# Kernel tuning notes

Measured on AMD Instinct MI355X. Metric: run time of the kernel, lower is better.

Reference implementation:

```python
import jax, jax.numpy as jnp
import numpy as np

NTYPES = 2
MAXNEI = 100
MNT = MAXNEI * NTYPES  # max_neighbor * ntypes = 200
RMIN = 0.5
RMAX = 6.0
M1 = 100   # last embedding width
M2 = 16
FH = 240   # fitting hidden width
NPHYS = 4
TFEAT = 8
B, NAT = 4, 1024


def mlp_resnet(x, Ws, bs):
    # DeepMD-style MLP: tanh layers with identity / duplicated-identity resnet
    for W, b in zip(Ws, bs):
        h = jnp.tanh(x @ W + b)
        if h.shape[-1] == x.shape[-1]:
            h = h + x
        elif h.shape[-1] == 2 * x.shape[-1]:
            h = h + jnp.concatenate([x, x], axis=-1)
        x = h
    return x


def setup_inputs() -> dict:
    key = jax.random.key(0)
    ks = jax.random.split(key, 24)
    r = jax.random.uniform(ks[0], (B, NAT, MNT), minval=0.1, maxval=7.0)
    pad = jax.random.uniform(ks[1], (B, NAT, MNT)) < 0.25
    r = jnp.where(pad, 0.0, r)
    d = jax.random.normal(ks[2], (B, NAT, MNT, 3))
    d = d / jnp.linalg.norm(d, axis=-1, keepdims=True)
    ImageDR = jnp.concatenate([r[..., None], r[..., None] * d], axis=-1).astype(jnp.float32)

    list_neigh = jax.random.randint(ks[3], (B, NAT, MNT), 0, MAXNEI)
    Imagetype_map = jax.random.randint(ks[4], (NAT,), 0, NTYPES).astype(jnp.int32)
    type_map = jnp.array([3, 14], dtype=jnp.int64)

    davg = (0.1 * jax.random.normal(ks[5], (NTYPES, MNT, 4))).astype(jnp.float32)
    dstd = (1.0 + 0.1 * jax.random.uniform(ks[6], (NTYPES, MNT, 4))).astype(jnp.float32)

    def w(k, shape):
        return (jax.random.normal(k, shape) / np.sqrt(shape[-2] if len(shape) > 1 else 1.0)).astype(jnp.float32)

    type_vector = jax.random.normal(ks[7], (NTYPES, NPHYS)).astype(jnp.float32)
    tW0 = w(ks[8], (NPHYS, TFEAT)); tb0 = jnp.zeros((TFEAT,), jnp.float32)
    eW0 = w(ks[9], (1 + TFEAT, 25)); eb0 = jnp.zeros((25,), jnp.float32)
    eW1 = w(ks[10], (25, 50));       eb1 = jnp.zeros((50,), jnp.float32)
    eW2 = w(ks[11], (50, M1));       eb2 = jnp.zeros((M1,), jnp.float32)
    fW0 = w(ks[12], (NTYPES, M2 * M1, FH)); fb0 = jnp.zeros((NTYPES, FH), jnp.float32)
    fW1 = w(ks[13], (NTYPES, FH, FH));      fb1 = jnp.zeros((NTYPES, FH), jnp.float32)
    fW2 = w(ks[14], (NTYPES, FH, FH));      fb2 = jnp.zeros((NTYPES, FH), jnp.float32)
    fWf = w(ks[15], (NTYPES, FH, 1))
    energy_shift = jnp.array([-3.2, -5.1], jnp.float32).reshape(NTYPES, 1)
    fbf = (0.01 * jax.random.normal(ks[16], (NTYPES, 1))).astype(jnp.float32) + energy_shift

    return dict(list_neigh=list_neigh, Imagetype_map=Imagetype_map, type_map=type_map,
                ImageDR=ImageDR, nghost=0, davg=davg, dstd=dstd, type_vector=type_vector,
                tW0=tW0, tb0=tb0, eW0=eW0, eb0=eb0, eW1=eW1, eb1=eb1, eW2=eW2, eb2=eb2,
                fW0=fW0, fb0=fb0, fW1=fW1, fb1=fb1, fW2=fW2, fb2=fb2, fWf=fWf, fbf=fbf)


def _forward(ImageDR, davg, dstd, type_vector, tW0, tb0, eW0, eb0, eW1, eb1, eW2, eb2,
             fW0, fb0, fW1, fb1, fW2, fb2, fWf, fbf, Imagetype_map):
    r = ImageDR[..., 0]
    r_safe = jnp.where(r > 1e-5, r, 1.0)
    inv_r = 1.0 / r_safe
    u = (r - RMIN) / (RMAX - RMIN)
    s_mid = inv_r * (u ** 3 * (-6.0 * u ** 2 + 15.0 * u - 10.0) + 1.0)
    Srij = jnp.where((r > 0) & (r < RMIN), inv_r,
                     jnp.where((r >= RMIN) & (r < RMAX), s_mid, 0.0))  # (B,N,J)
    mask = (jnp.abs(r) > 1e-5)[..., None]
    Ri = jnp.concatenate([Srij[..., None],
                          jnp.where(mask, Srij[..., None] * ImageDR[..., 1:4] * inv_r[..., None], 0.0)],
                         axis=-1)  # (B,N,J,4)
    # per-atom-type normalization
    Ri = (Ri - davg[Imagetype_map][None]) / dstd[Imagetype_map][None]

    # neighbor type feature from type-embedding net
    nt_idx = jnp.arange(MNT) // MAXNEI              # (J,) neighbor slot -> type
    tfeat = mlp_resnet(type_vector, [tW0], [tb0])   # (ntypes, TFEAT)
    nf = jnp.broadcast_to(tfeat[nt_idx][None, None], Ri.shape[:3] + (TFEAT,))
    x = jnp.concatenate([Ri[..., 0:1], nf], axis=-1)            # (B,N,J,1+TFEAT)
    G = mlp_resnet(x, [eW0, eW1, eW2], [eb0, eb1, eb2])         # (B,N,J,M1)

    xyz = jnp.einsum('bnjd,bnjm->bndm', Ri, G) / MNT            # (B,N,4,M1)
    DR = jnp.einsum('bndm,bndq->bnmq', xyz, xyz[..., :M2])      # (B,N,M1,M2)
    DR = DR.reshape(DR.shape[0], DR.shape[1], M1 * M2)

    Ei = jnp.zeros(DR.shape[:2], DR.dtype)
    for t in range(NTYPES):  # per-type fitting nets
        h = mlp_resnet(DR, [fW0[t], fW1[t], fW2[t]], [fb0[t], fb1[t], fb2[t]])
        e = (h @ fWf[t] + fbf[t])[..., 0]
        Ei = jnp.where(Imagetype_map[None, :] == t, e, Ei)
    Etot = jnp.sum(Ei, axis=1, keepdims=True)  # (B,1)
    return Etot, Ei


def reference(list_neigh, Imagetype_map, type_map, ImageDR, nghost, davg, dstd, type_vector,
              tW0, tb0, eW0, eb0, eW1, eb1, eW2, eb2,
              fW0, fb0, fW1, fb1, fW2, fb2, fWf, fbf):
    # list_neigh/type_map/nghost only participate in force computation (is_calc_f=False path)
    return _forward(ImageDR, davg, dstd, type_vector, tW0, tb0, eW0, eb0, eW1, eb1, eW2, eb2,
                    fW0, fb0, fW1, fb1, fW2, fb2, fWf, fbf, Imagetype_map)
```

## Files before the change

kernel.cpp:

```cpp
#include <hip/hip_runtime.h>
#include <hip/hip_bf16.h>

#define NATC  1024
#define BATCH 4
#define MNTC  200
#define M1C   100
#define M2C   16
#define FHC   240
#define KPAD  256
#define HSTR  264
#define H1STR 40
#define H2STR 72

typedef __attribute__((ext_vector_type(8))) short bf16x8;
typedef __attribute__((ext_vector_type(4))) float f32x4;

__device__ __forceinline__ float fast_tanh(float x){
    float e = __expf(2.0f * x);
    float r = __fdividef(1.0f, e + 1.0f);
    return fmaf(-2.0f, r, 1.0f);
}

__device__ __forceinline__ unsigned short f2bf(float x){
    __hip_bfloat16 h = __float2bfloat16(x);
    return *reinterpret_cast<unsigned short*>(&h);
}

__device__ __forceinline__ float bf2f(unsigned short u){
    unsigned int v = ((unsigned int)u) << 16;
    return *reinterpret_cast<float*>(&v);
}

__device__ __forceinline__ unsigned int pack2(float a, float b){
    return (unsigned int)f2bf(a) | ((unsigned int)f2bf(b) << 16);
}

__global__ __launch_bounds__(256) void part_kernel(const int* __restrict__ tmap,
                                                   int* __restrict__ idx,
                                                   int* __restrict__ counts){
    __shared__ int s0[256], s1[256];
    const int tid = threadIdx.x;
    int ty[4]; int c0 = 0, c1 = 0;
    #pragma unroll
    for (int r = 0; r < 4; ++r){
        ty[r] = tmap[tid*4 + r];
        if (ty[r] == 0) c0++; else c1++;
    }
    s0[tid] = c0; s1[tid] = c1;
    __syncthreads();
    for (int off = 1; off < 256; off <<= 1){
        int v0 = (tid >= off) ? s0[tid-off] : 0;
        int v1 = (tid >= off) ? s1[tid-off] : 0;
        __syncthreads();
        s0[tid] += v0; s1[tid] += v1;
        __syncthreads();
    }
    int e0 = s0[tid] - c0, e1 = s1[tid] - c1;
    #pragma unroll
    for (int r = 0; r < 4; ++r){
        int n = tid*4 + r;
        if (ty[r] == 0) idx[e0++] = n; else idx[NATC + e1++] = n;
    }
    if (tid == 255){ counts[0] = s0[255]; counts[1] = s1[255]; }
}

__global__ __launch_bounds__(256) void transp_kernel(const float* __restrict__ src,
                                                     unsigned short* __restrict__ dst,
                                                     int K, int N, int Kpad, int nkt, int nnt){
    __shared__ float tile[64][65];
    const int tid = threadIdx.x;
    int bid = blockIdx.x;
    const int t  = bid / (nkt*nnt);
    bid -= t*nkt*nnt;
    const int kt = bid / nnt;
    const int nt = bid - kt*nnt;
    const float* s = src + (size_t)t*K*N;
    unsigned short* d = dst + (size_t)t*N*Kpad;

    const int c  = tid & 63;
    const int rg = tid >> 6;
    #pragma unroll
    for (int p = 0; p < 16; ++p){
        int row = p*4 + rg;
        int gr = kt*64 + row, gc = nt*64 + c;
        tile[row][c] = (gr < K && gc < N) ? s[(size_t)gr*N + gc] : 0.0f;
    }
    __syncthreads();
    const int nn0 = tid >> 3;
    const int k8  = (tid & 7) * 8;
    #pragma unroll
    for (int p = 0; p < 2; ++p){
        int nn = p*32 + nn0;
        int gn = nt*64 + nn;
        int gk = kt*64 + k8;
        if (gn < N && gk < Kpad){
            unsigned short v[8];
            #pragma unroll
            for (int j = 0; j < 8; ++j) v[j] = f2bf(tile[k8+j][nn]);
            *(bf16x8*)(d + (size_t)gn*Kpad + gk) = *(bf16x8*)v;
        }
    }
}

__global__ __launch_bounds__(256) void prep_kernel(const float* __restrict__ tv,
                                                   const float* __restrict__ tW0,
                                                   const float* __restrict__ tb0,
                                                   const float* __restrict__ eW1,
                                                   const float* __restrict__ eW2,
                                                   unsigned short* __restrict__ ew1t,
                                                   unsigned short* __restrict__ ew2t,
                                                   float* __restrict__ tf_g){
    const int tid = threadIdx.x;
    if (tid < 16){
        int t = tid >> 3, f = tid & 7;
        float s = tb0[f];
        #pragma unroll
        for (int p = 0; p < 4; ++p) s = fmaf(tv[t*4+p], tW0[p*8+f], s);
        tf_g[tid] = fast_tanh(s) + tv[t*4 + (f & 3)];
    }
    for (int i = tid; i < 112*64; i += 256){
        int n = i >> 6, k = i & 63;
        ew2t[i] = (n < M1C && k < 50) ? f2bf(eW2[(size_t)k*M1C + n]) : (unsigned short)0;
    }
    for (int i = tid; i < 64*32; i += 256){
        int n = i >> 5, k = i & 31;
        ew1t[i] = (n < 50 && k < 25) ? f2bf(eW1[(size_t)k*50 + n]) : (unsigned short)0;
    }
}

__global__ __launch_bounds__(256, 2) void embed_kernel(
    const float4* __restrict__ imdr,
    const float4* __restrict__ davg,
    const float4* __restrict__ dstd,
    const int*    __restrict__ tmap,
    const float*  __restrict__ tf_g,
    const float*  __restrict__ eW0,
    const float*  __restrict__ eb0,
    const float*  __restrict__ eb1,
    const float*  __restrict__ eb2,
    const unsigned short* __restrict__ ew1t,
    const unsigned short* __restrict__ ew2t,
    unsigned short* __restrict__ DRout)
{
    __shared__ __align__(16) float Rif[256][4];
    __shared__ __align__(16) unsigned short H1s[256][H1STR];
    __shared__ __align__(16) unsigned short H2s[256][H2STR];

    const int tid = threadIdx.x;
    const int a   = blockIdx.x;
    const int n0  = a & (NATC - 1);
    const int itype = tmap[n0];
    const int j = tid;

    {
        unsigned int* rowp = (unsigned int*)&H1s[j][0];
        if (j < MNTC){
            float4 dr = imdr[(size_t)a*MNTC + j];
            float r  = dr.x;
            float rs = (r > 1e-5f) ? r : 1.0f;
            float ir = __fdividef(1.0f, rs);
            float u  = (r - 0.5f) * (1.0f/5.5f);
            float u2 = u*u, u3 = u2*u;
            float smid = ir * (u3 * (-6.0f*u2 + 15.0f*u - 10.0f) + 1.0f);
            float S = 0.0f;
            if (r > 0.0f && r < 0.5f)       S = ir;
            else if (r >= 0.5f && r < 6.0f) S = smid;
            bool msk = fabsf(r) > 1e-5f;
            float R0 = S;
            float R1 = msk ? S * dr.y * ir : 0.0f;
            float R2 = msk ? S * dr.z * ir : 0.0f;
            float R3 = msk ? S * dr.w * ir : 0.0f;
            float4 av = davg[itype*MNTC + j];
            float4 sv = dstd[itype*MNTC + j];
            float rin0 = __fdividef(R0 - av.x, sv.x);
            float rin1 = __fdividef(R1 - av.y, sv.y);
            float rin2 = __fdividef(R2 - av.z, sv.z);
            float rin3 = __fdividef(R3 - av.w, sv.w);
            Rif[j][0] = rin0; Rif[j][1] = rin1; Rif[j][2] = rin2; Rif[j][3] = rin3;

            float xf[8];
            const int tb = (j >= 100) ? 8 : 0;
            #pragma unroll
            for (int f = 0; f < 8; ++f) xf[f] = tf_g[tb + f];

            float h1[25];
            #pragma unroll
            for (int o = 0; o < 25; ++o) h1[o] = fmaf(rin0, eW0[o], eb0[o]);
            #pragma unroll
            for (int k = 0; k < 8; ++k){
                float hv = xf[k];
                #pragma unroll
                for (int o = 0; o < 25; ++o) h1[o] = fmaf(hv, eW0[(k+1)*25 + o], h1[o]);
            }
            #pragma unroll
            for (int o = 0; o < 25; ++o) h1[o] = fast_tanh(h1[o]);

            #pragma unroll
            for (int c = 0; c < 12; ++c) rowp[c] = pack2(h1[2*c], h1[2*c+1]);
            rowp[12] = (unsigned int)f2bf(h1[24]);
            #pragma unroll
            for (int c = 13; c < 20; ++c) rowp[c] = 0u;
        } else {
            Rif[j][0] = 0.0f; Rif[j][1] = 0.0f; Rif[j][2] = 0.0f; Rif[j][3] = 0.0f;
            #pragma unroll
            for (int c = 0; c < 20; ++c) rowp[c] = 0u;
        }
    }
    __syncthreads();

    const int lane = tid & 63;
    const int w    = tid >> 6;
    const int lc   = lane & 15;
    const int lg   = lane >> 4;

    #pragma unroll
    for (int mi = 0; mi < 4; ++mi){
        const int mt = w + mi*4;
        bf16x8 af = *(const bf16x8*)&H1s[mt*16 + lc][lg*8];
        const int rbase = mt*16 + lg*4;
        #pragma unroll
        for (int nt = 0; nt < 4; ++nt){
            const int n = nt*16 + lc;
            const bool live = (n < 50);
            float bv = live ? eb1[n] : 0.0f;
            f32x4 c;
            c[0] = bv; c[1] = bv; c[2] = bv; c[3] = bv;
            bf16x8 bfr = *(const bf16x8*)(ew1t + n*32 + lg*8);
            c = __builtin_amdgcn_mfma_f32_16x16x32_bf16(af, bfr, c, 0, 0, 0);
            const int rc = n % 25;
            #pragma unroll
            for (int i = 0; i < 4; ++i){
                const int row = rbase + i;
                unsigned short v = 0;
                if (live) v = f2bf(fast_tanh(c[i]) + bf2f(H1s[row][rc]));
                H2s[row][n] = v;
            }
        }
    }
    __syncthreads();

    float* xyzp = (float*)&H1s[0][0];
    float* xyzs = xyzp + 4*4*112;

    float bias[7];
    #pragma unroll
    for (int nt = 0; nt < 7; ++nt){
        int cg = nt*16 + lc;
        bias[nt] = (cg < M1C) ? eb2[cg] : 0.0f;
    }

    float xacc[7][4];
    #pragma unroll
    for (int nt = 0; nt < 7; ++nt)
        #pragma unroll
        for (int d = 0; d < 4; ++d) xacc[nt][d] = 0.0f;

    #pragma unroll
    for (int mi = 0; mi < 4; ++mi){
        const int mt = w + mi*4;
        const int rbase = mt*16 + lg*4;
        float4 rj[4];
        #pragma unroll
        for (int i = 0; i < 4; ++i) rj[i] = *(const float4*)&Rif[rbase + i][0];
        const unsigned short* arow = &H2s[mt*16 + lc][0];
        bf16x8 a0 = *(const bf16x8*)(arow + lg*8);
        bf16x8 a1 = *(const bf16x8*)(arow + 32 + lg*8);
        #pragma unroll
        for (int nt = 0; nt < 7; ++nt){
            const unsigned short* bp = ew2t + (size_t)(nt*16 + lc)*64 + lg*8;
            bf16x8 b0 = *(const bf16x8*)(bp);
            bf16x8 b1 = *(const bf16x8*)(bp + 32);
            f32x4 c;
            c[0] = bias[nt]; c[1] = bias[nt]; c[2] = bias[nt]; c[3] = bias[nt];
            c = __builtin_amdgcn_mfma_f32_16x16x32_bf16(a0, b0, c, 0, 0, 0);
            c = __builtin_amdgcn_mfma_f32_16x16x32_bf16(a1, b1, c, 0, 0, 0);
            const int cg = nt*16 + lc;
            const int rc = (cg >= 100) ? cg - 100 : ((cg >= 50) ? cg - 50 : cg);
            #pragma unroll
            for (int i = 0; i < 4; ++i){
                float g = fast_tanh(c[i]) + bf2f(H2s[rbase + i][rc]);
                xacc[nt][0] = fmaf(g, rj[i].x, xacc[nt][0]);
                xacc[nt][1] = fmaf(g, rj[i].y, xacc[nt][1]);
                xacc[nt][2] = fmaf(g, rj[i].z, xacc[nt][2]);
                xacc[nt][3] = fmaf(g, rj[i].w, xacc[nt][3]);
            }
        }
    }
    #pragma unroll
    for (int nt = 0; nt < 7; ++nt){
        #pragma unroll
        for (int d = 0; d < 4; ++d){
            float v = xacc[nt][d];
            v += __shfl_xor(v, 16);
            v += __shfl_xor(v, 32);
            if (lane < 16) xyzp[((w*4 + d)*112) + nt*16 + lc] = v;
        }
    }
    __syncthreads();

    for (int i = tid; i < 4*112; i += 256){
        int d = i / 112, m = i - d*112;
        xyzs[d*112 + m] = (xyzp[(0*4+d)*112 + m] + xyzp[(1*4+d)*112 + m] +
                           xyzp[(2*4+d)*112 + m] + xyzp[(3*4+d)*112 + m])
                          * (1.0f / (float)MNTC);
    }
    __syncthreads();

    for (int i = tid; i < M1C*M2C; i += 256){
        int m = i >> 4, q = i & 15;
        float s = 0.0f;
        #pragma unroll
        for (int d = 0; d < 4; ++d) s = fmaf(xyzs[d*112 + m], xyzs[d*112 + q], s);
        DRout[(size_t)a*(M1C*M2C) + i] = f2bf(s);
    }
}

__global__ __launch_bounds__(512) void fitm_kernel(
    const unsigned short* __restrict__ DRbf,
    const int*   __restrict__ idx,
    const int*   __restrict__ counts,
    const unsigned short* __restrict__ w0t,
    const unsigned short* __restrict__ w1t,
    const unsigned short* __restrict__ w2t,
    const float* __restrict__ fb0,
    const float* __restrict__ fb1,
    const float* __restrict__ fb2,
    const float* __restrict__ fWf,
    const float* __restrict__ fbf,
    float* __restrict__ out)
{
    const int bid = blockIdx.x;
    const int g = bid & 63;
    const int t = (bid >> 6) & 1;
    const int b = bid >> 7;
    const int cnt  = counts[t];
    const int base = g * 16;
    if (base >= cnt) return;
    const int na = min(16, cnt - base);

    __shared__ int ns[16];
    __shared__ __align__(16) unsigned short hA[16][HSTR];
    __shared__ __align__(16) unsigned short hB[16][HSTR];
    __shared__ float epart[8][16];

    const int tid  = threadIdx.x;
    const int lane = tid & 63;
    const int w    = tid >> 6;
    if (tid < 16) ns[tid] = idx[t*NATC + base + ((tid < na) ? tid : 0)];
    __syncthreads();

    const int lc = lane & 15;
    const int lg = lane >> 4;

    int   ncol[2];  bool act[2];  float bias0[2];
    #pragma unroll
    for (int nt = 0; nt < 2; ++nt){
        ncol[nt] = w*32 + nt*16 + lc;
        act[nt]  = (w*32 + nt*16) < FHC;
        bias0[nt] = act[nt] ? fb0[t*FHC + ncol[nt]] : 0.0f;
    }

    const unsigned short* aptr0 = DRbf + ((size_t)(b*NATC + ns[lc]))*1600 + lg*8;
    const unsigned short* bptr0[2];
    #pragma unroll
    for (int nt = 0; nt < 2; ++nt)
        bptr0[nt] = act[nt] ? (w0t + ((size_t)(t*FHC + ncol[nt]))*1600 + lg*8) : w0t;

    f32x4 acc[2];
    #pragma unroll
    for (int nt = 0; nt < 2; ++nt){
        acc[nt][0] = bias0[nt]; acc[nt][1] = bias0[nt];
        acc[nt][2] = bias0[nt]; acc[nt][3] = bias0[nt];
    }
    #pragma unroll 4
    for (int ks = 0; ks < 50; ++ks){
        bf16x8 af = *(const bf16x8*)(aptr0 + ks*32);
        #pragma unroll
        for (int nt = 0; nt < 2; ++nt){
            if (act[nt]){
                bf16x8 bfg = *(const bf16x8*)(bptr0[nt] + ks*32);
                acc[nt] = __builtin_amdgcn_mfma_f32_16x16x32_bf16(af, bfg, acc[nt], 0, 0, 0);
            }
        }
    }
    float h0r[2][4];
    #pragma unroll
    for (int nt = 0; nt < 2; ++nt){
        #pragma unroll
        for (int i = 0; i < 4; ++i){
            int row = lg*4 + i;
            if (act[nt]){
                h0r[nt][i] = fast_tanh(acc[nt][i]);
                hA[row][ncol[nt]] = f2bf(h0r[nt][i]);
            } else {
                h0r[nt][i] = 0.0f;
                hA[row][ncol[nt]] = 0;
            }
        }
    }
    __syncthreads();

    f32x4 acc1[2];
    #pragma unroll
    for (int nt = 0; nt < 2; ++nt){
        float bv = act[nt] ? fb1[t*FHC + ncol[nt]] : 0.0f;
        acc1[nt][0] = bv; acc1[nt][1] = bv; acc1[nt][2] = bv; acc1[nt][3] = bv;
    }
    const unsigned short* b1p[2];
    #pragma unroll
    for (int nt = 0; nt < 2; ++nt)
        b1p[nt] = act[nt] ? (w1t + ((size_t)(t*FHC + ncol[nt]))*KPAD + lg*8) : w1t;
    #pragma unroll
    for (int ks = 0; ks < 8; ++ks){
        bf16x8 af = *(const bf16x8*)&hA[lc][ks*32 + lg*8];
        #pragma unroll
        for (int nt = 0; nt < 2; ++nt){
            if (act[nt]){
                bf16x8 bfg = *(const bf16x8*)(b1p[nt] + ks*32);
                acc1[nt] = __builtin_amdgcn_mfma_f32_16x16x32_bf16(af, bfg, acc1[nt], 0, 0, 0);
            }
        }
    }
    float h1r[2][4];
    #pragma unroll
    for (int nt = 0; nt < 2; ++nt){
        #pragma unroll
        for (int i = 0; i < 4; ++i){
            int row = lg*4 + i;
            if (act[nt]){
                h1r[nt][i] = fast_tanh(acc1[nt][i]) + h0r[nt][i];
                hB[row][ncol[nt]] = f2bf(h1r[nt][i]);
            } else {
                h1r[nt][i] = 0.0f;
                hB[row][ncol[nt]] = 0;
            }
        }
    }
    __syncthreads();

    f32x4 acc2[2];
    #pragma unroll
    for (int nt = 0; nt < 2; ++nt){
        float bv = act[nt] ? fb2[t*FHC + ncol[nt]] : 0.0f;
        acc2[nt][0] = bv; acc2[nt][1] = bv; acc2[nt][2] = bv; acc2[nt][3] = bv;
    }
    const unsigned short* b2p[2];
    #pragma unroll
    for (int nt = 0; nt < 2; ++nt)
        b2p[nt] = act[nt] ? (w2t + ((size_t)(t*FHC + ncol[nt]))*KPAD + lg*8) : w2t;
    #pragma unroll
    for (int ks = 0; ks < 8; ++ks){
        bf16x8 af = *(const bf16x8*)&hB[lc][ks*32 + lg*8];
        #pragma unroll
        for (int nt = 0; nt < 2; ++nt){
            if (act[nt]){
                bf16x8 bfg = *(const bf16x8*)(b2p[nt] + ks*32);
                acc2[nt] = __builtin_amdgcn_mfma_f32_16x16x32_bf16(af, bfg, acc2[nt], 0, 0, 0);
            }
        }
    }

    float p0 = 0.0f, p1 = 0.0f, p2 = 0.0f, p3 = 0.0f;
    #pragma unroll
    for (int nt = 0; nt < 2; ++nt){
        if (act[nt]){
            float wfv = fWf[t*FHC + ncol[nt]];
            float h;
            h = fast_tanh(acc2[nt][0]) + h1r[nt][0]; p0 = fmaf(h, wfv, p0);
            h = fast_tanh(acc2[nt][1]) + h1r[nt][1]; p1 = fmaf(h, wfv, p1);
            h = fast_tanh(acc2[nt][2]) + h1r[nt][2]; p2 = fmaf(h, wfv, p2);
            h = fast_tanh(acc2[nt][3]) + h1r[nt][3]; p3 = fmaf(h, wfv, p3);
        }
    }
    #pragma unroll
    for (int off = 1; off < 16; off <<= 1){
        p0 += __shfl_xor(p0, off);
        p1 += __shfl_xor(p1, off);
        p2 += __shfl_xor(p2, off);
        p3 += __shfl_xor(p3, off);
    }
    if (lc == 0){
        epart[w][lg*4 + 0] = p0;
        epart[w][lg*4 + 1] = p1;
        epart[w][lg*4 + 2] = p2;
        epart[w][lg*4 + 3] = p3;
    }
    __syncthreads();
    if (tid < 16){
        float e = fbf[t];
        #pragma unroll
        for (int ww = 0; ww < 8; ++ww) e += epart[ww][tid];
        float ee = 0.0f;
        if (tid < na){
            out[4 + b*NATC + ns[tid]] = e;
            ee = e;
        }
        #pragma unroll
        for (int off = 8; off >= 1; off >>= 1) ee += __shfl_down(ee, off, 16);
        if (tid == 0) atomicAdd(&out[b], ee);
    }
}

extern "C" void kernel_launch(void* const* d_in, const int* in_sizes, int n_in,
                              void* d_out, int out_size, void* d_ws, size_t ws_size,
                              hipStream_t stream)
{
    (void)in_sizes; (void)n_in; (void)out_size; (void)ws_size;
    const int*   tmap = (const int*)d_in[1];
    const float* imdr = (const float*)d_in[3];
    const float* davg = (const float*)d_in[5];
    const float* dstd = (const float*)d_in[6];
    const float* tv   = (const float*)d_in[7];
    const float* tW0  = (const float*)d_in[8];
    const float* tb0  = (const float*)d_in[9];
    const float* eW0  = (const float*)d_in[10];
    const float* eb0  = (const float*)d_in[11];
    const float* eW1  = (const float*)d_in[12];
    const float* eb1  = (const float*)d_in[13];
    const float* eW2  = (const float*)d_in[14];
    const float* eb2  = (const float*)d_in[15];
    const float* fW0  = (const float*)d_in[16];
    const float* fb0  = (const float*)d_in[17];
    const float* fW1  = (const float*)d_in[18];
    const float* fb1  = (const float*)d_in[19];
    const float* fW2  = (const float*)d_in[20];
    const float* fb2  = (const float*)d_in[21];
    const float* fWf  = (const float*)d_in[22];
    const float* fbf  = (const float*)d_in[23];
    float* out = (float*)d_out;

    char* ws = (char*)d_ws;
    int*   counts = (int*)ws;
    int*   idx    = (int*)(ws + 64);
    unsigned short* DRbf = (unsigned short*)(ws + 16384);
    unsigned short* w0t  = DRbf + (size_t)BATCH*NATC*1600;
    unsigned short* w1t  = w0t + (size_t)2*FHC*1600;
    unsigned short* w2t  = w1t + (size_t)2*FHC*KPAD;
    unsigned short* ew2t = w2t + (size_t)2*FHC*KPAD;
    unsigned short* ew1t = ew2t + 112*64;
    float* tf_g          = (float*)(ew1t + 64*32);

    hipMemsetAsync(d_out, 0, 4*sizeof(float), stream);
    part_kernel<<<1, 256, 0, stream>>>(tmap, idx, counts);
    prep_kernel<<<1, 256, 0, stream>>>(tv, tW0, tb0, eW1, eW2, ew1t, ew2t, tf_g);
    transp_kernel<<<2*25*4, 256, 0, stream>>>(fW0, w0t, 1600, FHC, 1600, 25, 4);
    transp_kernel<<<2*4*4,  256, 0, stream>>>(fW1, w1t, FHC, FHC, KPAD, 4, 4);
    transp_kernel<<<2*4*4,  256, 0, stream>>>(fW2, w2t, FHC, FHC, KPAD, 4, 4);
    embed_kernel<<<BATCH*NATC, 256, 0, stream>>>(
        (const float4*)imdr, (const float4*)davg, (const float4*)dstd, tmap,
        tf_g, eW0, eb0, eb1, eb2, ew1t, ew2t, DRbf);
    fitm_kernel<<<512, 512, 0, stream>>>(
        DRbf, idx, counts, w0t, w1t, w2t, fb0, fb1, fb2, fWf, fbf, out);
}
```

Measured before the change: 413.9 us.

## Precompute type-embedding bias, split embed accumulators, vectorize DR store, halve fitting tiles

The per-type contribution of the type features to the first embedding layer is folded into a precomputed bias table in the prep kernel, so each neighbor thread does one FMA and a tanh per output instead of nine FMAs. The second embedding GEMM epilogue is split into two halves to cut live accumulator registers. The DR outer product now writes eight bf16 values per thread with a vector store. The fitting kernel processes 8 atoms per block with twice as many blocks, which wastes half of each 16-row MFMA tile in exchange for more parallelism.

New measurement: 485.9 us. 17.4% more time.

```diff
diff --git a/kernel.cpp b/kernel.cpp
--- a/kernel.cpp
+++ b/kernel.cpp
@@ -105,18 +105,33 @@
 __global__ __launch_bounds__(256) void prep_kernel(const float* __restrict__ tv,
                                                    const float* __restrict__ tW0,
                                                    const float* __restrict__ tb0,
+                                                   const float* __restrict__ eW0,
+                                                   const float* __restrict__ eb0,
                                                    const float* __restrict__ eW1,
                                                    const float* __restrict__ eW2,
                                                    unsigned short* __restrict__ ew1t,
                                                    unsigned short* __restrict__ ew2t,
-                                                   float* __restrict__ tf_g){
+                                                   float* __restrict__ Tb){
+    __shared__ float tfl[16];
     const int tid = threadIdx.x;
     if (tid < 16){
         int t = tid >> 3, f = tid & 7;
         float s = tb0[f];
         #pragma unroll
         for (int p = 0; p < 4; ++p) s = fmaf(tv[t*4+p], tW0[p*8+f], s);
-        tf_g[tid] = fast_tanh(s) + tv[t*4 + (f & 3)];
+        tfl[tid] = fast_tanh(s) + tv[t*4 + (f & 3)];
+    }
+    __syncthreads();
+    if (tid < 64){
+        int t = tid >> 5, o = tid & 31;
+        if (o < 25){
+            float s = eb0[o];
+            #pragma unroll
+            for (int k = 0; k < 8; ++k) s = fmaf(tfl[t*8 + k], eW0[(k+1)*25 + o], s);
+            Tb[t*32 + o] = s;
+        } else {
+            Tb[t*32 + o] = 0.0f;
+        }
     }
     for (int i = tid; i < 112*64; i += 256){
         int n = i >> 6, k = i & 63;
@@ -133,9 +148,8 @@
     const float4* __restrict__ davg,
     const float4* __restrict__ dstd,
     const int*    __restrict__ tmap,
-    const float*  __restrict__ tf_g,
     const float*  __restrict__ eW0,
-    const float*  __restrict__ eb0,
+    const float*  __restrict__ Tb,
     const float*  __restrict__ eb1,
     const float*  __restrict__ eb2,
     const unsigned short* __restrict__ ew1t,
@@ -178,22 +192,11 @@
             float rin3 = __fdividef(R3 - av.w, sv.w);
             Rif[j][0] = rin0; Rif[j][1] = rin1; Rif[j][2] = rin2; Rif[j][3] = rin3;
 
-            float xf[8];
-            const int tb = (j >= 100) ? 8 : 0;
-            #pragma unroll
-            for (int f = 0; f < 8; ++f) xf[f] = tf_g[tb + f];
-
+            const float* tb = Tb + ((j >= 100) ? 32 : 0);
             float h1[25];
             #pragma unroll
-            for (int o = 0; o < 25; ++o) h1[o] = fmaf(rin0, eW0[o], eb0[o]);
-            #pragma unroll
-            for (int k = 0; k < 8; ++k){
-                float hv = xf[k];
-                #pragma unroll
-                for (int o = 0; o < 25; ++o) h1[o] = fmaf(hv, eW0[(k+1)*25 + o], h1[o]);
-            }
-            #pragma unroll
-            for (int o = 0; o < 25; ++o) h1[o] = fast_tanh(h1[o]);
+            for (int o = 0; o < 25; ++o)
+                h1[o] = fast_tanh(fmaf(rin0, eW0[o], tb[o]));
 
             #pragma unroll
             for (int c = 0; c < 12; ++c) rowp[c] = pack2(h1[2*c], h1[2*c+1]);
@@ -242,58 +245,60 @@
     float* xyzp = (float*)&H1s[0][0];
     float* xyzs = xyzp + 4*4*112;
 
-    float bias[7];
-    #pragma unroll
-    for (int nt = 0; nt < 7; ++nt){
-        int cg = nt*16 + lc;
-        bias[nt] = (cg < M1C) ? eb2[cg] : 0.0f;
-    }
-
-    float xacc[7][4];
-    #pragma unroll
-    for (int nt = 0; nt < 7; ++nt)
-        #pragma unroll
-        for (int d = 0; d < 4; ++d) xacc[nt][d] = 0.0f;
-
-    #pragma unroll
-    for (int mi = 0; mi < 4; ++mi){
-        const int mt = w + mi*4;
-        const int rbase = mt*16 + lg*4;
-        float4 rj[4];
-        #pragma unroll
-        for (int i = 0; i < 4; ++i) rj[i] = *(const float4*)&Rif[rbase + i][0];
-        const unsigned short* arow = &H2s[mt*16 + lc][0];
-        bf16x8 a0 = *(const bf16x8*)(arow + lg*8);
-        bf16x8 a1 = *(const bf16x8*)(arow + 32 + lg*8);
-        #pragma unroll
-        for (int nt = 0; nt < 7; ++nt){
-            const unsigned short* bp = ew2t + (size_t)(nt*16 + lc)*64 + lg*8;
-            bf16x8 b0 = *(const bf16x8*)(bp);
-            bf16x8 b1 = *(const bf16x8*)(bp + 32);
-            f32x4 c;
-            c[0] = bias[nt]; c[1] = bias[nt]; c[2] = bias[nt]; c[3] = bias[nt];
-            c = __builtin_amdgcn_mfma_f32_16x16x32_bf16(a0, b0, c, 0, 0, 0);
-            c = __builtin_amdgcn_mfma_f32_16x16x32_bf16(a1, b1, c, 0, 0, 0);
-            const int cg = nt*16 + lc;
-            const int rc = (cg >= 100) ? cg - 100 : ((cg >= 50) ? cg - 50 : cg);
-            #pragma unroll
-            for (int i = 0; i < 4; ++i){
-                float g = fast_tanh(c[i]) + bf2f(H2s[rbase + i][rc]);
-                xacc[nt][0] = fmaf(g, rj[i].x, xacc[nt][0]);
-                xacc[nt][1] = fmaf(g, rj[i].y, xacc[nt][1]);
-                xacc[nt][2] = fmaf(g, rj[i].z, xacc[nt][2]);
-                xacc[nt][3] = fmaf(g, rj[i].w, xacc[nt][3]);
-            }
-        }
-    }
-    #pragma unroll
-    for (int nt = 0; nt < 7; ++nt){
-        #pragma unroll
-        for (int d = 0; d < 4; ++d){
-            float v = xacc[nt][d];
-            v += __shfl_xor(v, 16);
-            v += __shfl_xor(v, 32);
-            if (lane < 16) xyzp[((w*4 + d)*112) + nt*16 + lc] = v;
+    #pragma unroll
+    for (int half = 0; half < 2; ++half){
+        const int ntbase = half * 4;
+        float xacc[4][4];
+        #pragma unroll
+        for (int q = 0; q < 4; ++q)
+            #pragma unroll
+            for (int d = 0; d < 4; ++d) xacc[q][d] = 0.0f;
+
+        #pragma unroll
+        for (int mi = 0; mi < 4; ++mi){
+            const int mt = w + mi*4;
+            const int rbase = mt*16 + lg*4;
+            float4 rj[4];
+            #pragma unroll
+            for (int i = 0; i < 4; ++i) rj[i] = *(const float4*)&Rif[rbase + i][0];
+            const unsigned short* arow = &H2s[mt*16 + lc][0];
+            bf16x8 a0 = *(const bf16x8*)(arow + lg*8);
+            bf16x8 a1 = *(const bf16x8*)(arow + 32 + lg*8);
+            #pragma unroll
+            for (int q = 0; q < 4; ++q){
+                const int nt = ntbase + q;
+                if (nt >= 7) continue;
+                const int cg = nt*16 + lc;
+                const unsigned short* bp = ew2t + (size_t)cg*64 + lg*8;
+                bf16x8 b0 = *(const bf16x8*)(bp);
+                bf16x8 b1 = *(const bf16x8*)(bp + 32);
+                float bv = (cg < M1C) ? eb2[cg] : 0.0f;
+                f32x4 c;
+                c[0] = bv; c[1] = bv; c[2] = bv; c[3] = bv;
+                c = __builtin_amdgcn_mfma_f32_16x16x32_bf16(a0, b0, c, 0, 0, 0);
+                c = __builtin_amdgcn_mfma_f32_16x16x32_bf16(a1, b1, c, 0, 0, 0);
+                const int rc = (cg >= 100) ? cg - 100 : ((cg >= 50) ? cg - 50 : cg);
+                #pragma unroll
+                for (int i = 0; i < 4; ++i){
+                    float g = fast_tanh(c[i]) + bf2f(H2s[rbase + i][rc]);
+                    xacc[q][0] = fmaf(g, rj[i].x, xacc[q][0]);
+                    xacc[q][1] = fmaf(g, rj[i].y, xacc[q][1]);
+                    xacc[q][2] = fmaf(g, rj[i].z, xacc[q][2]);
+                    xacc[q][3] = fmaf(g, rj[i].w, xacc[q][3]);
+                }
+            }
+        }
+        #pragma unroll
+        for (int q = 0; q < 4; ++q){
+            const int nt = ntbase + q;
+            if (nt >= 7) continue;
+            #pragma unroll
+            for (int d = 0; d < 4; ++d){
+                float v = xacc[q][d];
+                v += __shfl_xor(v, 16);
+                v += __shfl_xor(v, 32);
+                if (lane < 16) xyzp[((w*4 + d)*112) + nt*16 + lc] = v;
+            }
         }
     }
     __syncthreads();
@@ -306,12 +311,24 @@
     }
     __syncthreads();
 
-    for (int i = tid; i < M1C*M2C; i += 256){
-        int m = i >> 4, q = i & 15;
-        float s = 0.0f;
-        #pragma unroll
-        for (int d = 0; d < 4; ++d) s = fmaf(xyzs[d*112 + m], xyzs[d*112 + q], s);
-        DRout[(size_t)a*(M1C*M2C) + i] = f2bf(s);
+    if (tid < 200){
+        const int i8 = tid * 8;
+        const int m  = i8 >> 4;
+        const int qb = i8 & 15;
+        float xm[4], s[8];
+        #pragma unroll
+        for (int d = 0; d < 4; ++d) xm[d] = xyzs[d*112 + m];
+        #pragma unroll
+        for (int e = 0; e < 8; ++e){
+            float acc = 0.0f;
+            #pragma unroll
+            for (int d = 0; d < 4; ++d) acc = fmaf(xm[d], xyzs[d*112 + qb + e], acc);
+            s[e] = acc;
+        }
+        unsigned short v[8];
+        #pragma unroll
+        for (int e = 0; e < 8; ++e) v[e] = f2bf(s[e]);
+        *(bf16x8*)(DRout + (size_t)a*(M1C*M2C) + i8) = *(bf16x8*)v;
     }
 }
 
@@ -330,15 +347,15 @@
     float* __restrict__ out)
 {
     const int bid = blockIdx.x;
-    const int g = bid & 63;
-    const int t = (bid >> 6) & 1;
-    const int b = bid >> 7;
+    const int g = bid & 127;
+    const int t = (bid >> 7) & 1;
+    const int b = bid >> 8;
     const int cnt  = counts[t];
-    const int base = g * 16;
+    const int base = g * 8;
     if (base >= cnt) return;
-    const int na = min(16, cnt - base);
-
-    __shared__ int ns[16];
+    const int na = min(8, cnt - base);
+
+    __shared__ int ns[8];
     __shared__ __align__(16) unsigned short hA[16][HSTR];
     __shared__ __align__(16) unsigned short hB[16][HSTR];
     __shared__ float epart[8][16];
@@ -346,7 +363,7 @@
     const int tid  = threadIdx.x;
     const int lane = tid & 63;
     const int w    = tid >> 6;
-    if (tid < 16) ns[tid] = idx[t*NATC + base + ((tid < na) ? tid : 0)];
+    if (tid < 8) ns[tid] = idx[t*NATC + base + ((tid < na) ? tid : 0)];
     __syncthreads();
 
     const int lc = lane & 15;
@@ -360,7 +377,7 @@
         bias0[nt] = act[nt] ? fb0[t*FHC + ncol[nt]] : 0.0f;
     }
 
-    const unsigned short* aptr0 = DRbf + ((size_t)(b*NATC + ns[lc]))*1600 + lg*8;
+    const unsigned short* aptr0 = DRbf + ((size_t)(b*NATC + ns[lc & 7]))*1600 + lg*8;
     const unsigned short* bptr0[2];
     #pragma unroll
     for (int nt = 0; nt < 2; ++nt)
@@ -486,7 +503,7 @@
         epart[w][lg*4 + 3] = p3;
     }
     __syncthreads();
-    if (tid < 16){
+    if (tid < 8){
         float e = fbf[t];
         #pragma unroll
         for (int ww = 0; ww < 8; ++ww) e += epart[ww][tid];
@@ -496,7 +513,7 @@
             ee = e;
         }
         #pragma unroll
-        for (int off = 8; off >= 1; off >>= 1) ee += __shfl_down(ee, off, 16);
+        for (int off = 4; off >= 1; off >>= 1) ee += __shfl_down(ee, off, 8);
         if (tid == 0) atomicAdd(&out[b], ee);
     }
 }
@@ -538,17 +555,17 @@
     unsigned short* w2t  = w1t + (size_t)2*FHC*KPAD;
     unsigned short* ew2t = w2t + (size_t)2*FHC*KPAD;
     unsigned short* ew1t = ew2t + 112*64;
-    float* tf_g          = (float*)(ew1t + 64*32);
+    float* Tb            = (float*)(ew1t + 64*32);
 
     hipMemsetAsync(d_out, 0, 4*sizeof(float), stream);
     part_kernel<<<1, 256, 0, stream>>>(tmap, idx, counts);
-    prep_kernel<<<1, 256, 0, stream>>>(tv, tW0, tb0, eW1, eW2, ew1t, ew2t, tf_g);
+    prep_kernel<<<1, 256, 0, stream>>>(tv, tW0, tb0, eW0, eb0, eW1, eW2, ew1t, ew2t, Tb);
     transp_kernel<<<2*25*4, 256, 0, stream>>>(fW0, w0t, 1600, FHC, 1600, 25, 4);
     transp_kernel<<<2*4*4,  256, 0, stream>>>(fW1, w1t, FHC, FHC, KPAD, 4, 4);
     transp_kernel<<<2*4*4,  256, 0, stream>>>(fW2, w2t, FHC, FHC, KPAD, 4, 4);
     embed_kernel<<<BATCH*NATC, 256, 0, stream>>>(
         (const float4*)imdr, (const float4*)davg, (const float4*)dstd, tmap,
-        tf_g, eW0, eb0, eb1, eb2, ew1t, ew2t, DRbf);
-    fitm_kernel<<<512, 512, 0, stream>>>(
+        eW0, Tb, eb1, eb2, ew1t, ew2t, DRbf);
+    fitm_kernel<<<1024, 512, 0, stream>>>(
         DRbf, idx, counts, w0t, w1t, w2t, fb0, fb1, fb2, fWf, fbf, out);
 }
```
